# Performance work log

Measured on AMD Instinct MI355X. Metric: run time of the kernel, lower is better.

## Reference

```python
import jax, jax.numpy as jnp
import numpy as np

B, S, D, H = 2, 2048, 1024, 16
DK = D // H


def setup_inputs() -> dict:
    key = jax.random.key(0)
    ks = jax.random.split(key, 11)
    scale = 1.0 / np.sqrt(D)
    inp = {
        "q": jax.random.normal(ks[0], (B, S, D), jnp.float32),
        "k": jax.random.normal(ks[1], (B, S, D), jnp.float32),
        "v": jax.random.normal(ks[2], (B, S, D), jnp.float32),
        "mask": jnp.tril(jnp.ones((S, S), jnp.int32))[None, None],  # causal [1,1,S,S]
        "wq": jax.random.normal(ks[3], (D, D), jnp.float32) * scale,
        "bq": jnp.zeros((D,), jnp.float32),
        "wk": jax.random.normal(ks[4], (D, D), jnp.float32) * scale,
        "bk": jnp.zeros((D,), jnp.float32),
        "wv": jax.random.normal(ks[5], (D, D), jnp.float32) * scale,
        "bv": jnp.zeros((D,), jnp.float32),
        "wo": jax.random.normal(ks[6], (D, D), jnp.float32) * scale,
        "bo": jnp.zeros((D,), jnp.float32),
    }
    return inp


def _split_heads(x):  # [B,S,D] -> [B,H,S,DK]
    return x.reshape(B, S, H, DK).transpose(0, 2, 1, 3)


def reference(q, k, v, mask, wq, bq, wk, bk, wv, bv, wo, bo):
    # projections (nn.Linear: x @ W.T + b)
    query = _split_heads(q @ wq.T + bq)
    key_ = _split_heads(k @ wk.T + bk)
    value = _split_heads(v @ wv.T + bv)
    # scaled dot-product attention, full [B,H,S,S] scores as in source
    scores = jnp.einsum('bhqd,bhkd->bhqk', query, key_) / np.sqrt(DK)
    scores = jnp.where(mask == 0, jnp.float32(-1e9), scores)
    attn = jax.nn.softmax(scores, axis=-1)
    out = jnp.einsum('bhqk,bhkd->bhqd', attn, value)
    out = out.transpose(0, 2, 1, 3).reshape(B, S, D)
    x = out @ wo.T + bo
    return x, attn
```

## Files before the change

kernel.cpp:

```cpp
#include <hip/hip_runtime.h>
#include <hip/hip_bf16.h>

typedef __attribute__((ext_vector_type(8))) __bf16 bf16x8;
typedef __attribute__((ext_vector_type(4))) __bf16 bf16x4;
typedef __attribute__((ext_vector_type(4))) float f32x4;

#define MFMA16(a, b, c) __builtin_amdgcn_mfma_f32_16x16x32_bf16((a), (b), (c), 0, 0, 0)

#define SEQ 2048
#define DIM 1024

__device__ __forceinline__ void gload_lds16(const __bf16* g, __bf16* l) {
  __builtin_amdgcn_global_load_lds(
      (const __attribute__((address_space(1))) void*)g,
      (__attribute__((address_space(3))) void*)l, 16, 0, 0);
}

__global__ __launch_bounds__(256) void cvt_bf16(
    const float* __restrict__ q, const float* __restrict__ k, const float* __restrict__ v,
    const float* __restrict__ wq, const float* __restrict__ wk, const float* __restrict__ wv,
    const float* __restrict__ wo,
    __bf16* __restrict__ qb, __bf16* __restrict__ kb, __bf16* __restrict__ vb,
    __bf16* __restrict__ wqb, __bf16* __restrict__ wkb, __bf16* __restrict__ wvb,
    __bf16* __restrict__ wob) {
  int a = blockIdx.y;
  const float* src = (a == 0) ? q : (a == 1) ? k : (a == 2) ? v
                    : (a == 3) ? wq : (a == 4) ? wk : (a == 5) ? wv : wo;
  __bf16* dst = (a == 0) ? qb : (a == 1) ? kb : (a == 2) ? vb
               : (a == 3) ? wqb : (a == 4) ? wkb : (a == 5) ? wvb : wob;
  size_t n = (a < 3) ? (size_t)(2 * SEQ * DIM) : (size_t)(DIM * DIM);
  size_t i = ((size_t)blockIdx.x * 256 + threadIdx.x) * 8;
  if (i >= n) return;
  float4 f0 = *(const float4*)&src[i];
  float4 f1 = *(const float4*)&src[i + 4];
  bf16x8 o = {(__bf16)f0.x, (__bf16)f0.y, (__bf16)f0.z, (__bf16)f0.w,
              (__bf16)f1.x, (__bf16)f1.y, (__bf16)f1.z, (__bf16)f1.w};
  *(bf16x8*)&dst[i] = o;
}

__global__ __launch_bounds__(256) void qkv_gemm(
    const __bf16* __restrict__ qI, const __bf16* __restrict__ kI, const __bf16* __restrict__ vI,
    const __bf16* __restrict__ wqI, const __bf16* __restrict__ wkI, const __bf16* __restrict__ wvI,
    const float* __restrict__ bqI, const float* __restrict__ bkI, const float* __restrict__ bvI,
    __bf16* __restrict__ Qp, __bf16* __restrict__ Kp, __bf16* __restrict__ Vt) {
  const int N = 1024, K = 1024;
  int z = blockIdx.z;
  const __bf16* A = (z == 0) ? qI : (z == 1) ? kI : vI;
  const __bf16* W = (z == 0) ? wqI : (z == 1) ? wkI : wvI;
  const float* bias = (z == 0) ? bqI : (z == 1) ? bkI : bvI;

  __shared__ __bf16 As[2][128 * 32];
  __shared__ __bf16 Bs[2][128 * 32];

  int tid = threadIdx.x;
  int wave = tid >> 6, lane = tid & 63;
  int quad = lane >> 4, l16 = lane & 15;
  int wm = (wave >> 1) * 64, wn = (wave & 1) * 64;
  int m0 = blockIdx.y * 128, n0 = blockIdx.x * 128;

  int srow = wave * 16 + (lane >> 2);
  int scol = (lane & 3) * 8;
  const __bf16* Ab = &A[(size_t)(m0 + srow) * K + scol];
  const __bf16* Wb = &W[(size_t)(n0 + srow) * K + scol];
  int lo = wave * 512;

  f32x4 acc[4][4] = {};

  {
    gload_lds16(Ab, &As[0][lo]);
    gload_lds16(Ab + (size_t)64 * K, &As[0][lo + 2048]);
    gload_lds16(Wb, &Bs[0][lo]);
    gload_lds16(Wb + (size_t)64 * K, &Bs[0][lo + 2048]);
  }

  int buf = 0;
  for (int k0 = 0; k0 < K; k0 += 32) {
    __syncthreads();
    if (k0 + 32 < K) {
      int nb = buf ^ 1;
      gload_lds16(Ab + k0 + 32, &As[nb][lo]);
      gload_lds16(Ab + (size_t)64 * K + k0 + 32, &As[nb][lo + 2048]);
      gload_lds16(Wb + k0 + 32, &Bs[nb][lo]);
      gload_lds16(Wb + (size_t)64 * K + k0 + 32, &Bs[nb][lo + 2048]);
    }
    const __bf16* as = &As[buf][0];
    const __bf16* bs = &Bs[buf][0];
    bf16x8 af[4], bfv[4];
#pragma unroll
    for (int i = 0; i < 4; i++) af[i] = *(const bf16x8*)&as[(wm + i * 16 + l16) * 32 + quad * 8];
#pragma unroll
    for (int j = 0; j < 4; j++) bfv[j] = *(const bf16x8*)&bs[(wn + j * 16 + l16) * 32 + quad * 8];
#pragma unroll
    for (int i = 0; i < 4; i++)
#pragma unroll
      for (int j = 0; j < 4; j++) acc[i][j] = MFMA16(af[i], bfv[j], acc[i][j]);
    buf ^= 1;
  }

#pragma unroll
  for (int j = 0; j < 4; j++) {
    int col = n0 + wn + j * 16 + l16;
    float bj = bias[col];
    if (z == 2) {
#pragma unroll
      for (int i = 0; i < 4; i++) {
        int row0 = m0 + wm + i * 16 + quad * 4;
        int bb = row0 >> 11, s = row0 & 2047;
        bf16x4 pv = {(__bf16)(acc[i][j][0] + bj), (__bf16)(acc[i][j][1] + bj),
                     (__bf16)(acc[i][j][2] + bj), (__bf16)(acc[i][j][3] + bj)};
        *(bf16x4*)&Vt[((size_t)bb * 1024 + col) * SEQ + s] = pv;
      }
    } else {
      __bf16* C = (z == 0) ? Qp : Kp;
      float scale = (z == 0) ? 0.125f : 1.0f;
#pragma unroll
      for (int i = 0; i < 4; i++)
#pragma unroll
        for (int r = 0; r < 4; r++) {
          int row = m0 + wm + i * 16 + quad * 4 + r;
          C[(size_t)row * N + col] = (__bf16)((acc[i][j][r] + bj) * scale);
        }
    }
  }
}

__global__ __launch_bounds__(256) void out_gemm(
    const __bf16* __restrict__ A, const __bf16* __restrict__ W,
    const float* __restrict__ bias, float* __restrict__ C) {
  const int N = 1024, K = 1024;
  __shared__ __bf16 As[2][128 * 32];
  __shared__ __bf16 Bs[2][128 * 32];

  int tid = threadIdx.x;
  int wave = tid >> 6, lane = tid & 63;
  int quad = lane >> 4, l16 = lane & 15;
  int wm = (wave >> 1) * 64, wn = (wave & 1) * 64;
  int m0 = blockIdx.y * 128, n0 = blockIdx.x * 128;

  int srow = wave * 16 + (lane >> 2);
  int scol = (lane & 3) * 8;
  const __bf16* Ab = &A[(size_t)(m0 + srow) * K + scol];
  const __bf16* Wb = &W[(size_t)(n0 + srow) * K + scol];
  int lo = wave * 512;

  f32x4 acc[4][4] = {};

  {
    gload_lds16(Ab, &As[0][lo]);
    gload_lds16(Ab + (size_t)64 * K, &As[0][lo + 2048]);
    gload_lds16(Wb, &Bs[0][lo]);
    gload_lds16(Wb + (size_t)64 * K, &Bs[0][lo + 2048]);
  }

  int buf = 0;
  for (int k0 = 0; k0 < K; k0 += 32) {
    __syncthreads();
    if (k0 + 32 < K) {
      int nb = buf ^ 1;
      gload_lds16(Ab + k0 + 32, &As[nb][lo]);
      gload_lds16(Ab + (size_t)64 * K + k0 + 32, &As[nb][lo + 2048]);
      gload_lds16(Wb + k0 + 32, &Bs[nb][lo]);
      gload_lds16(Wb + (size_t)64 * K + k0 + 32, &Bs[nb][lo + 2048]);
    }
    const __bf16* as = &As[buf][0];
    const __bf16* bs = &Bs[buf][0];
    bf16x8 af[4], bfv[4];
#pragma unroll
    for (int i = 0; i < 4; i++) af[i] = *(const bf16x8*)&as[(wm + i * 16 + l16) * 32 + quad * 8];
#pragma unroll
    for (int j = 0; j < 4; j++) bfv[j] = *(const bf16x8*)&bs[(wn + j * 16 + l16) * 32 + quad * 8];
#pragma unroll
    for (int i = 0; i < 4; i++)
#pragma unroll
      for (int j = 0; j < 4; j++) acc[i][j] = MFMA16(af[i], bfv[j], acc[i][j]);
    buf ^= 1;
  }

#pragma unroll
  for (int j = 0; j < 4; j++) {
    int col = n0 + wn + j * 16 + l16;
    float bj = bias[col];
#pragma unroll
    for (int i = 0; i < 4; i++)
#pragma unroll
      for (int r = 0; r < 4; r++) {
        int row = m0 + wm + i * 16 + quad * 4 + r;
        C[(size_t)row * N + col] = acc[i][j][r] + bj;
      }
  }
}

__global__ __launch_bounds__(256) void attn_fused(
    const __bf16* __restrict__ Qp, const __bf16* __restrict__ Kp,
    const __bf16* __restrict__ Vt, float* __restrict__ attn,
    __bf16* __restrict__ Oc) {
  int bh = blockIdx.y;
  int b = bh >> 4;
  int hofs = (bh & 15) * 64;
  int q0 = (31 - blockIdx.x) * 64;

  int tid = threadIdx.x;
  int wave = tid >> 6, lane = tid & 63;
  int quad = lane >> 4, l16 = lane & 15;

  __shared__ __bf16 Ks[128][72];
  __shared__ __bf16 Vts[64][136];
  __shared__ __bf16 Ps[64][136];

  const size_t rowbase = (size_t)b * SEQ;
  const size_t vtbase = (size_t)bh * 64 * SEQ;

  int qg = q0 + wave * 16 + l16;

  const __bf16* qpp = &Qp[(rowbase + qg) * DIM + hofs + quad * 8];
  bf16x8 qfrag0 = *(const bf16x8*)qpp;
  bf16x8 qfrag1 = *(const bf16x8*)(qpp + 32);

  float m_i = -1e30f, l_i = 0.f;
  int ktmax = (q0 + 63) >> 7;

  for (int kt = 0; kt <= ktmax; kt++) {
    int k0 = kt << 7;
    __syncthreads();
#pragma unroll
    for (int it = 0; it < 4; it++) {
      int flat = tid * 8 + it * 2048;
      int r = flat >> 6, c = flat & 63;
      *(bf16x8*)&Ks[r][c] = *(const bf16x8*)&Kp[(rowbase + k0 + r) * DIM + hofs + c];
    }
    __syncthreads();

    f32x4 sacc[8] = {};
#pragma unroll
    for (int t = 0; t < 8; t++) {
      bf16x8 a0 = *(bf16x8*)&Ks[t * 16 + l16][quad * 8];
      bf16x8 a1 = *(bf16x8*)&Ks[t * 16 + l16][32 + quad * 8];
      sacc[t] = MFMA16(a0, qfrag0, sacc[t]);
      sacc[t] = MFMA16(a1, qfrag1, sacc[t]);
    }

    bool diag = (kt == ktmax);
    float sv[32];
    float mx = -1e30f;
#pragma unroll
    for (int t = 0; t < 8; t++)
#pragma unroll
      for (int r = 0; r < 4; r++) {
        float s = sacc[t][r];
        int k = k0 + t * 16 + quad * 4 + r;
        if (diag && k > qg) s = -1e30f;
        sv[t * 4 + r] = s;
        mx = fmaxf(mx, s);
      }
    mx = fmaxf(mx, __shfl_xor(mx, 16));
    mx = fmaxf(mx, __shfl_xor(mx, 32));
    float mn = fmaxf(m_i, mx);
    float sum = 0.f;
#pragma unroll
    for (int i = 0; i < 32; i++) sum += __expf(sv[i] - mn);
    sum += __shfl_xor(sum, 16);
    sum += __shfl_xor(sum, 32);
    l_i = l_i * __expf(m_i - mn) + sum;
    m_i = mn;
  }

  float rl = 1.f / l_i;
  f32x4 oacc[4] = {};
  float* attn_bh = attn + (size_t)bh * SEQ * SEQ;
  float* attn_row = attn_bh + (size_t)qg * SEQ;

  for (int kt = 0; kt < SEQ / 128; kt++) {
    int k0 = kt << 7;
    if (kt <= ktmax) {
      __syncthreads();
#pragma unroll
      for (int it = 0; it < 4; it++) {
        int flat = tid * 8 + it * 2048;
        int r = flat >> 6, c = flat & 63;
        *(bf16x8*)&Ks[r][c] = *(const bf16x8*)&Kp[(rowbase + k0 + r) * DIM + hofs + c];
        int d = flat >> 7, c2 = flat & 127;
        *(bf16x8*)&Vts[d][c2] = *(const bf16x8*)&Vt[vtbase + (size_t)d * SEQ + k0 + c2];
      }
      __syncthreads();

      f32x4 sacc[8] = {};
#pragma unroll
      for (int t = 0; t < 8; t++) {
        bf16x8 a0 = *(bf16x8*)&Ks[t * 16 + l16][quad * 8];
        bf16x8 a1 = *(bf16x8*)&Ks[t * 16 + l16][32 + quad * 8];
        sacc[t] = MFMA16(a0, qfrag0, sacc[t]);
        sacc[t] = MFMA16(a1, qfrag1, sacc[t]);
      }

      bool diag = (kt == ktmax);
#pragma unroll
      for (int t = 0; t < 8; t++) {
        float p[4];
#pragma unroll
        for (int r = 0; r < 4; r++) {
          int k = k0 + t * 16 + quad * 4 + r;
          float s = sacc[t][r];
          p[r] = (!diag || k <= qg) ? __expf(s - m_i) * rl : 0.f;
        }
        *(float4*)&attn_row[k0 + t * 16 + quad * 4] = make_float4(p[0], p[1], p[2], p[3]);
        bf16x4 ph = {(__bf16)p[0], (__bf16)p[1], (__bf16)p[2], (__bf16)p[3]};
        *(bf16x4*)&Ps[wave * 16 + l16][t * 16 + quad * 4] = ph;
      }
      asm volatile("s_waitcnt lgkmcnt(0)" ::: "memory");

#pragma unroll
      for (int ks = 0; ks < 4; ks++) {
        bf16x8 a = *(bf16x8*)&Ps[wave * 16 + l16][ks * 32 + quad * 8];
#pragma unroll
        for (int dt = 0; dt < 4; dt++) {
          bf16x8 bb = *(bf16x8*)&Vts[dt * 16 + l16][ks * 32 + quad * 8];
          oacc[dt] = MFMA16(a, bb, oacc[dt]);
        }
      }
    } else {
      float4 z4 = make_float4(0.f, 0.f, 0.f, 0.f);
#pragma unroll
      for (int i = 0; i < 8; i++) {
        int f4 = tid + i * 256;
        int r = f4 >> 5;
        int c = (f4 & 31) * 4;
        *(float4*)&attn_bh[(size_t)(q0 + r) * SEQ + k0 + c] = z4;
      }
    }
  }

#pragma unroll
  for (int dt = 0; dt < 4; dt++)
#pragma unroll
    for (int rr = 0; rr < 4; rr++) {
      int row = q0 + wave * 16 + quad * 4 + rr;
      Oc[(rowbase + row) * DIM + hofs + dt * 16 + l16] = (__bf16)oacc[dt][rr];
    }
}

extern "C" void kernel_launch(void* const* d_in, const int* in_sizes, int n_in,
                              void* d_out, int out_size, void* d_ws, size_t ws_size,
                              hipStream_t stream) {
  const float* q = (const float*)d_in[0];
  const float* k = (const float*)d_in[1];
  const float* v = (const float*)d_in[2];
  const float* wq = (const float*)d_in[4];
  const float* bq = (const float*)d_in[5];
  const float* wk = (const float*)d_in[6];
  const float* bk = (const float*)d_in[7];
  const float* wv = (const float*)d_in[8];
  const float* bv = (const float*)d_in[9];
  const float* wo = (const float*)d_in[10];
  const float* bo = (const float*)d_in[11];

  float* xout = (float*)d_out;
  float* attn = xout + (size_t)2 * SEQ * DIM;

  const size_t NBS = (size_t)2 * SEQ * DIM;
  const size_t NW = (size_t)DIM * DIM;

  __bf16* Qp = (__bf16*)d_ws;
  __bf16* Kp = Qp + NBS;
  __bf16* Vt = Kp + NBS;
  __bf16* Oc = Vt + NBS;
  __bf16* qb = Oc + NBS;
  __bf16* kb = qb + NBS;
  __bf16* vb = kb + NBS;
  __bf16* wqb = vb + NBS;
  __bf16* wkb = wqb + NW;
  __bf16* wvb = wkb + NW;
  __bf16* wob = wvb + NW;

  dim3 blk(256);

  dim3 g0(2048, 7);
  cvt_bf16<<<g0, blk, 0, stream>>>(q, k, v, wq, wk, wv, wo,
                                   qb, kb, vb, wqb, wkb, wvb, wob);

  dim3 g1(8, 32, 3);
  qkv_gemm<<<g1, blk, 0, stream>>>(qb, kb, vb, wqb, wkb, wvb, bq, bk, bv, Qp, Kp, Vt);

  dim3 g2(32, 32);
  attn_fused<<<g2, blk, 0, stream>>>(Qp, Kp, Vt, attn, Oc);

  dim3 g3(8, 32);
  out_gemm<<<g3, blk, 0, stream>>>(Oc, wob, bo, xout);
}
```

Baseline: 767.7 us.

## Split fused attention into separate row-stats and output passes

The single attention kernel, which first computed the softmax max and sum and then recomputed the scores to write probabilities and the output, is split into two kernels. The first writes per-row max and reciprocal sum to a workspace buffer, and the second reads them back. The aim is smaller kernels with less shared memory and fewer registers, giving higher occupancy, in particular for the stats pass that no longer allocates V and P tiles. The cost is an extra launch plus a global round trip for the stats, and Q is loaded twice.

```diff
diff --git a/kernel.cpp b/kernel.cpp
--- a/kernel.cpp
+++ b/kernel.cpp
@@ -190,10 +190,9 @@
   }
 }
 
-__global__ __launch_bounds__(256) void attn_fused(
+__global__ __launch_bounds__(256) void attn_pass1(
     const __bf16* __restrict__ Qp, const __bf16* __restrict__ Kp,
-    const __bf16* __restrict__ Vt, float* __restrict__ attn,
-    __bf16* __restrict__ Oc) {
+    float2* __restrict__ ml) {
   int bh = blockIdx.y;
   int b = bh >> 4;
   int hofs = (bh & 15) * 64;
@@ -204,12 +203,8 @@
   int quad = lane >> 4, l16 = lane & 15;
 
   __shared__ __bf16 Ks[128][72];
-  __shared__ __bf16 Vts[64][136];
-  __shared__ __bf16 Ps[64][136];
 
   const size_t rowbase = (size_t)b * SEQ;
-  const size_t vtbase = (size_t)bh * 64 * SEQ;
-
   int qg = q0 + wave * 16 + l16;
 
   const __bf16* qpp = &Qp[(rowbase + qg) * DIM + hofs + quad * 8];
@@ -264,7 +259,39 @@
     m_i = mn;
   }
 
-  float rl = 1.f / l_i;
+  if (quad == 0) ml[(size_t)bh * SEQ + qg] = make_float2(m_i, 1.f / l_i);
+}
+
+__global__ __launch_bounds__(256) void attn_pass2(
+    const __bf16* __restrict__ Qp, const __bf16* __restrict__ Kp,
+    const __bf16* __restrict__ Vt, const float2* __restrict__ ml,
+    float* __restrict__ attn, __bf16* __restrict__ Oc) {
+  int bh = blockIdx.y;
+  int b = bh >> 4;
+  int hofs = (bh & 15) * 64;
+  int q0 = (31 - blockIdx.x) * 64;
+
+  int tid = threadIdx.x;
+  int wave = tid >> 6, lane = tid & 63;
+  int quad = lane >> 4, l16 = lane & 15;
+
+  __shared__ __bf16 Ks[128][72];
+  __shared__ __bf16 Vts[64][136];
+  __shared__ __bf16 Ps[64][136];
+
+  const size_t rowbase = (size_t)b * SEQ;
+  const size_t vtbase = (size_t)bh * 64 * SEQ;
+
+  int qg = q0 + wave * 16 + l16;
+
+  const __bf16* qpp = &Qp[(rowbase + qg) * DIM + hofs + quad * 8];
+  bf16x8 qfrag0 = *(const bf16x8*)qpp;
+  bf16x8 qfrag1 = *(const bf16x8*)(qpp + 32);
+
+  float2 st = ml[(size_t)bh * SEQ + qg];
+  float m_i = st.x, rl = st.y;
+
+  int ktmax = (q0 + 63) >> 7;
   f32x4 oacc[4] = {};
   float* attn_bh = attn + (size_t)bh * SEQ * SEQ;
   float* attn_row = attn_bh + (size_t)qg * SEQ;
@@ -370,6 +397,7 @@
   __bf16* wkb = wqb + NW;
   __bf16* wvb = wkb + NW;
   __bf16* wob = wvb + NW;
+  float2* ml = (float2*)(wob + NW);
 
   dim3 blk(256);
 
@@ -381,7 +409,8 @@
   qkv_gemm<<<g1, blk, 0, stream>>>(qb, kb, vb, wqb, wkb, wvb, bq, bk, bv, Qp, Kp, Vt);
 
   dim3 g2(32, 32);
-  attn_fused<<<g2, blk, 0, stream>>>(Qp, Kp, Vt, attn, Oc);
+  attn_pass1<<<g2, blk, 0, stream>>>(Qp, Kp, ml);
+  attn_pass2<<<g2, blk, 0, stream>>>(Qp, Kp, Vt, ml, attn, Oc);
 
   dim3 g3(8, 32);
   out_gemm<<<g3, blk, 0, stream>>>(Oc, wob, bo, xout);
```

New measurement: 782.2 us. No clear change (+1.9%).
